# Kernel optimization log

Measured on AMD Instinct MI355X. Metric: run time of the kernel, lower is better.

Reference implementation:

```python
import jax, jax.numpy as jnp
import numpy as np

D_MODEL = 768
N_HEADS = 8
HEAD_DIM = D_MODEL // N_HEADS
LN_EPS = 1e-5

def setup_inputs() -> dict:
    key = jax.random.key(0)
    k1, k2, k3 = jax.random.split(key, 3)
    B, L = 8, 4096
    x = jax.random.normal(k1, (B, L, D_MODEL), dtype=jnp.float32)
    gamma = jnp.ones((D_MODEL,), dtype=jnp.float32)
    beta = jnp.zeros((D_MODEL,), dtype=jnp.float32)
    # torch Linear weights transposed so forward is x @ W
    w_qkv = jax.random.normal(k2, (D_MODEL, 3 * D_MODEL), dtype=jnp.float32) * (1.0 / np.sqrt(D_MODEL))
    w_out = jax.random.normal(k3, (D_MODEL, D_MODEL), dtype=jnp.float32) * (1.0 / np.sqrt(D_MODEL))
    return {"x": x, "gamma": gamma, "beta": beta, "w_qkv": w_qkv, "w_out": w_out}

def reference(x, gamma, beta, w_qkv, w_out):
    B, L, D = x.shape
    residual = x
    # LayerNorm
    mu = jnp.mean(x, axis=-1, keepdims=True)
    var = jnp.mean(jnp.square(x - mu), axis=-1, keepdims=True)
    xn = (x - mu) * jax.lax.rsqrt(var + LN_EPS) * gamma + beta
    # qkv projection, split, reshape to [B, H, L, d]
    qkv = xn @ w_qkv  # [B, L, 3D]
    q, k, v = jnp.split(qkv, 3, axis=-1)
    def to_heads(t):
        return t.reshape(B, L, N_HEADS, HEAD_DIM).transpose(0, 2, 1, 3)
    q, k, v = to_heads(q), to_heads(k), to_heads(v)
    # feature maps: elu + 1
    q = jax.nn.elu(q) + 1.0
    k = jax.nn.elu(k) + 1.0
    # linear attention: kv aggregation then query readout
    kv = jnp.einsum('bhld,bhlv->bhdv', k, v)          # [B,H,d,d]
    out = jnp.einsum('bhld,bhdv->bhlv', q, kv)         # [B,H,L,d]
    k_sum = jnp.sum(k, axis=2)                         # [B,H,d]
    normalizer = jnp.einsum('bhld,bhd->bhl', q, k_sum) # [B,H,L]
    normalizer = jnp.maximum(normalizer, 1e-6)
    out = out / normalizer[..., None]
    out = out.transpose(0, 2, 1, 3).reshape(B, L, D)
    out = out @ w_out
    return out + residual
```

## Files before the change

kernel.cpp:

```cpp
#include <hip/hip_runtime.h>
#include <stdint.h>

#define D_MODEL 768
#define N3      2304
#define NHEAD   8
#define DH      96
#define BATCH   8
#define SEQ     4096
#define ROWS    (BATCH*SEQ)
#define LN_EPS  1e-5f

typedef __attribute__((ext_vector_type(8))) __bf16 bf16x8;
typedef __attribute__((ext_vector_type(4))) float f32x4;
typedef __attribute__((ext_vector_type(8))) unsigned short ushort8;
typedef __attribute__((ext_vector_type(4))) unsigned short ushort4v;

__device__ __forceinline__ unsigned short f2bf(float f) {
  union { float f; unsigned int u; } v; v.f = f;
  unsigned int r = v.u + 0x7FFFu + ((v.u >> 16) & 1u);
  return (unsigned short)(r >> 16);
}
__device__ __forceinline__ float bf2f(unsigned short u) {
  union { unsigned int u; float f; } v; v.u = ((unsigned int)u) << 16;
  return v.f;
}

#define GLOBAL_LDS16(src, dst) \
  __builtin_amdgcn_global_load_lds((const __attribute__((address_space(1))) void*)(src), \
                                   (__attribute__((address_space(3))) void*)(dst), 16, 0, 0)

#define GATE(n) do { asm volatile("s_waitcnt vmcnt(" #n ")" ::: "memory"); \
                     __builtin_amdgcn_s_barrier(); asm volatile("" ::: "memory"); } while (0)

__global__ __launch_bounds__(256) void transpose2_kernel(
    const float* __restrict__ wqkv, const float* __restrict__ wout,
    unsigned short* __restrict__ wqkvT, unsigned short* __restrict__ woutT) {
  __shared__ float tile[32][33];
  int bx = blockIdx.x;
  const float* in; unsigned short* out; int C, c0;
  if (bx < 72) { in = wqkv; out = wqkvT; C = N3;      c0 = bx * 32; }
  else         { in = wout; out = woutT; C = D_MODEL; c0 = (bx - 72) * 32; }
  int r0 = blockIdx.y * 32;
  int tx = threadIdx.x & 31, ty = threadIdx.x >> 5;
  #pragma unroll
  for (int i = ty; i < 32; i += 8)
    tile[i][tx] = in[(size_t)(r0 + i) * C + c0 + tx];
  __syncthreads();
  #pragma unroll
  for (int i = ty; i < 32; i += 8)
    out[(size_t)(c0 + i) * D_MODEL + r0 + tx] = f2bf(tile[tx][i]);
}

__global__ __launch_bounds__(256) void ln_kernel(
    const float* __restrict__ x, const float* __restrict__ gamma,
    const float* __restrict__ beta, unsigned short* __restrict__ xn) {
  int wave = threadIdx.x >> 6, lane = threadIdx.x & 63;
  int row = blockIdx.x * 4 + wave;
  const float* xr = x + (size_t)row * D_MODEL;
  f32x4 v[3];
  float s = 0.f, sq = 0.f;
  #pragma unroll
  for (int i = 0; i < 3; ++i) {
    v[i] = *(const f32x4*)(xr + (i * 64 + lane) * 4);
    #pragma unroll
    for (int c = 0; c < 4; ++c) { s += v[i][c]; sq += v[i][c] * v[i][c]; }
  }
  #pragma unroll
  for (int o = 32; o; o >>= 1) {
    s  += __shfl_xor(s, o, 64);
    sq += __shfl_xor(sq, o, 64);
  }
  float mu  = s * (1.f / 768.f);
  float var = sq * (1.f / 768.f) - mu * mu;
  float rs  = rsqrtf(var + LN_EPS);
  #pragma unroll
  for (int i = 0; i < 3; ++i) {
    int col = (i * 64 + lane) * 4;
    ushort4v o;
    #pragma unroll
    for (int c = 0; c < 4; ++c)
      o[c] = f2bf((v[i][c] - mu) * rs * gamma[col + c] + beta[col + c]);
    *(ushort4v*)(xn + (size_t)row * D_MODEL + col) = o;
  }
}

__global__ __launch_bounds__(256, 2) void gemm_qkv_w_kernel(
    const unsigned short* __restrict__ A, const unsigned short* __restrict__ Bt,
    unsigned short* __restrict__ qb, unsigned short* __restrict__ kT,
    unsigned short* __restrict__ vT) {
  __shared__ unsigned short As[3 * 4096];
  __shared__ unsigned short Bs[3 * 8192];
  const int K = D_MODEL, nbn = 9;
  int nwg = gridDim.x, id = blockIdx.x;
  int q8 = nwg >> 3;
  int wg = (id & 7) * q8 + (id >> 3);
  int bm = wg / nbn, bn = wg % nbn;

  const int lane = threadIdx.x & 63, wid = threadIdx.x >> 6;
  const int wn = wid;
  const int l15 = lane & 15, hi = lane >> 4;
  const int colS = (hi ^ ((l15 >> 1) & 3)) << 3;
  const int srow = lane >> 2;
  const int scol = ((lane & 3) ^ ((lane >> 3) & 3)) << 3;

  const unsigned short* a0 = A  + (size_t)(bm * 128 +      wid * 16 + srow) * K + scol;
  const unsigned short* a1 = A  + (size_t)(bm * 128 + 64 + wid * 16 + srow) * K + scol;
  const unsigned short* b0 = Bt + (size_t)(bn * 256 + wid * 64 +      srow) * K + scol;
  const unsigned short* b1 = Bt + (size_t)(bn * 256 + wid * 64 + 16 + srow) * K + scol;
  const unsigned short* b2 = Bt + (size_t)(bn * 256 + wid * 64 + 32 + srow) * K + scol;
  const unsigned short* b3 = Bt + (size_t)(bn * 256 + wid * 64 + 48 + srow) * K + scol;
  auto stage = [&](int buf, int kt) {
    GLOBAL_LDS16(a0 + kt * 32, &As[buf * 4096 +        wid * 512]);
    GLOBAL_LDS16(a1 + kt * 32, &As[buf * 4096 + 2048 + wid * 512]);
    GLOBAL_LDS16(b0 + kt * 32, &Bs[buf * 8192 + wid * 2048]);
    GLOBAL_LDS16(b1 + kt * 32, &Bs[buf * 8192 + wid * 2048 + 512]);
    GLOBAL_LDS16(b2 + kt * 32, &Bs[buf * 8192 + wid * 2048 + 1024]);
    GLOBAL_LDS16(b3 + kt * 32, &Bs[buf * 8192 + wid * 2048 + 1536]);
  };

  f32x4 acc[8][4];
  #pragma unroll
  for (int i = 0; i < 8; ++i)
    #pragma unroll
    for (int j = 0; j < 4; ++j) acc[i][j] = (f32x4){0.f, 0.f, 0.f, 0.f};

#define QTILE(BUF, STG) do { \
    bf16x8 af[8], bv[4]; \
    _Pragma("unroll") for (int mf = 0; mf < 8; ++mf) \
      af[mf] = *(const bf16x8*)&As[(BUF) * 4096 + (mf * 16 + l15) * 32 + colS]; \
    _Pragma("unroll") for (int nf = 0; nf < 4; ++nf) \
      bv[nf] = *(const bf16x8*)&Bs[(BUF) * 8192 + (wn * 64 + nf * 16 + l15) * 32 + colS]; \
    STG; \
    __builtin_amdgcn_s_setprio(1); \
    _Pragma("unroll") for (int mf = 0; mf < 8; ++mf) \
      _Pragma("unroll") for (int nf = 0; nf < 4; ++nf) \
        acc[mf][nf] = __builtin_amdgcn_mfma_f32_16x16x32_bf16( \
            af[mf], bv[nf], acc[mf][nf], 0, 0, 0); \
    __builtin_amdgcn_s_setprio(0); \
  } while (0)

  stage(0, 0); stage(1, 1);
  for (int it = 0; it < 7; ++it) {
    int T = 3 * it;
    GATE(6); QTILE(0, stage(2, T + 2));
    GATE(6); QTILE(1, stage(0, T + 3));
    GATE(6); QTILE(2, stage(1, T + 4));
  }
  GATE(6); QTILE(0, stage(2, 23));
  GATE(6); QTILE(1, {});
  GATE(0); QTILE(2, {});
#undef QTILE

  int r0 = bm * 128, c0 = bn * 256 + wn * 64;
  if (bn < 3) {
    #pragma unroll
    for (int mf = 0; mf < 8; ++mf)
      #pragma unroll
      for (int nf = 0; nf < 4; ++nf) {
        int col = c0 + nf * 16 + l15;
        #pragma unroll
        for (int r = 0; r < 4; ++r) {
          int row = r0 + mf * 16 + hi * 4 + r;
          float v = acc[mf][nf][r];
          v = (v > 0.f) ? v + 1.f : __expf(v);
          qb[(size_t)row * D_MODEL + col] = f2bf(v);
        }
      }
  } else {
    const bool isK = (bn < 6);
    unsigned short* T = isK ? kT : vT;
    int cbase = c0 - (isK ? 768 : 1536);
    #pragma unroll
    for (int mf = 0; mf < 8; ++mf) {
      int ll = mf * 16 + hi * 4;
      #pragma unroll
      for (int nf = 0; nf < 4; ++nf) {
        int cc = cbase + nf * 16 + l15;
        int h = cc / 96, d = cc - h * 96;
        ushort4v pk;
        #pragma unroll
        for (int r = 0; r < 4; ++r) {
          float v = acc[mf][nf][r];
          if (isK) v = (v > 0.f) ? v + 1.f : __expf(v);
          pk[r] = f2bf(v);
        }
        *(ushort4v*)&T[(((size_t)bm * 8 + h) * 96 + d) * 128 + ll] = pk;
      }
    }
  }
}

__global__ __launch_bounds__(256) void kvagg2_kernel(
    const unsigned short* __restrict__ kT, const unsigned short* __restrict__ vT,
    float* __restrict__ kvp) {
  __shared__ unsigned short KTs[3 * 6144];
  __shared__ unsigned short VTs[3 * 8192];
  int bh = blockIdx.x >> 2, chunk = blockIdx.x & 3;
  int tid = threadIdx.x;
  int lane = tid & 63, wid = tid >> 6;
  int l15 = lane & 15, hi = lane >> 4;

  #pragma unroll
  for (int i = 0; i < 3; ++i) {
    int s = i * 256 + tid;
    int buf = s >> 8, r = 96 + ((s >> 3) & 31), sl = s & 7;
    unsigned short val = (r == 96) ? (unsigned short)0x3F80 : (unsigned short)0;
    ushort8 v8 = {val, val, val, val, val, val, val, val};
    *(ushort8*)&VTs[buf * 8192 + r * 64 + sl * 8] = v8;
  }
  __syncthreads();

  const int b = bh >> 3, h = bh & 7;
  auto stage = [&](int buf, int t) {
    #pragma unroll
    for (int i = 0; i < 3; ++i) {
      int sidx = i * 256 + tid;
      int row = sidx >> 3;
      int L = (sidx & 7) ^ (row & 7);
      size_t g = ((((size_t)b * 32 + chunk * 8 + (t >> 1)) * 8 + h) * 96 + row) * 128
               + (t & 1) * 64 + L * 8;
      GLOBAL_LDS16(kT + g, &KTs[buf * 6144 + (i * 256 + wid * 64) * 8]);
      GLOBAL_LDS16(vT + g, &VTs[buf * 8192 + (i * 256 + wid * 64) * 8]);
    }
  };

  f32x4 acc[6][2];
  #pragma unroll
  for (int i = 0; i < 6; ++i)
    #pragma unroll
    for (int j = 0; j < 2; ++j) acc[i][j] = (f32x4){0.f, 0.f, 0.f, 0.f};

#define KVTILE(BUF) do { \
    _Pragma("unroll") for (int kq = 0; kq < 2; ++kq) { \
      bf16x8 af[6], bv[2]; \
      _Pragma("unroll") for (int mf = 0; mf < 6; ++mf) { \
        int row = mf * 16 + l15; \
        af[mf] = *(const bf16x8*)&KTs[(BUF) * 6144 + row * 64 + ((kq * 4 + hi) ^ (row & 7)) * 8]; } \
      _Pragma("unroll") for (int nf = 0; nf < 2; ++nf) { \
        int row = wid * 32 + nf * 16 + l15; \
        bv[nf] = *(const bf16x8*)&VTs[(BUF) * 8192 + row * 64 + ((kq * 4 + hi) ^ (row & 7)) * 8]; } \
      __builtin_amdgcn_s_setprio(1); \
      _Pragma("unroll") for (int mf = 0; mf < 6; ++mf) \
        _Pragma("unroll") for (int nf = 0; nf < 2; ++nf) \
          acc[mf][nf] = __builtin_amdgcn_mfma_f32_16x16x32_bf16( \
              af[mf], bv[nf], acc[mf][nf], 0, 0, 0); \
      __builtin_amdgcn_s_setprio(0); \
    } } while (0)

  stage(0, 0); stage(1, 1);
  for (int t = 0; t < 14; ++t) {
    stage((t + 2) % 3, t + 2);
    GATE(12);
    KVTILE(t % 3);
  }
  GATE(6); KVTILE(2);
  GATE(0); KVTILE(0);
#undef KVTILE

  float* outp = kvp + ((size_t)bh * 4 + chunk) * (96 * 112);
  #pragma unroll
  for (int nf = 0; nf < 2; ++nf) {
    int e = wid * 32 + nf * 16 + l15;
    if (e < 112) {
      #pragma unroll
      for (int mf = 0; mf < 6; ++mf)
        #pragma unroll
        for (int r = 0; r < 4; ++r) {
          int d = mf * 16 + hi * 4 + r;
          outp[d * 112 + e] = acc[mf][nf][r];
        }
    }
  }
}

__global__ __launch_bounds__(256) void kvreduce2_kernel(
    const float* __restrict__ kvp, unsigned short* __restrict__ kvN,
    float* __restrict__ ksumf) {
  int idx = blockIdx.x * 256 + threadIdx.x;
  if (idx >= 64 * 96 * 112) return;
  int e = idx % 112;
  int d = (idx / 112) % 96;
  int bh = idx / (112 * 96);
  float s = 0.f;
  #pragma unroll
  for (int c = 0; c < 4; ++c)
    s += kvp[(((size_t)bh * 4 + c) * 96 + d) * 112 + e];
  if (e < 96)       kvN[((size_t)bh * 96 + d) * 96 + e] = f2bf(s);
  else if (e == 96) ksumf[(size_t)bh * 96 + d] = s;
}

__global__ __launch_bounds__(256) void mpre_kernel(
    const unsigned short* __restrict__ kvN, const unsigned short* __restrict__ woutT,
    unsigned short* __restrict__ Mt) {
  int bx = blockIdx.x;
  int cb = bx % 3, h = (bx / 3) % 8, b = bx / 24;
  int bh = b * 8 + h;
  const int lane = threadIdx.x & 63, wid = threadIdx.x >> 6;
  const int l15 = lane & 15, hi = lane >> 4;

  f32x4 acc[6][4];
  #pragma unroll
  for (int i = 0; i < 6; ++i)
    #pragma unroll
    for (int j = 0; j < 4; ++j) acc[i][j] = (f32x4){0.f, 0.f, 0.f, 0.f};

  #pragma unroll
  for (int kq = 0; kq < 3; ++kq) {
    int e = kq * 32 + hi * 8;
    bf16x8 af[6], bv[4];
    #pragma unroll
    for (int rf = 0; rf < 6; ++rf) {
      int d = rf * 16 + l15;
      af[rf] = *(const bf16x8*)&kvN[((size_t)bh * 96 + d) * 96 + e];
    }
    #pragma unroll
    for (int cf = 0; cf < 4; ++cf) {
      int c = cb * 256 + wid * 64 + cf * 16 + l15;
      bv[cf] = *(const bf16x8*)&woutT[(size_t)c * 768 + h * 96 + e];
    }
    #pragma unroll
    for (int rf = 0; rf < 6; ++rf)
      #pragma unroll
      for (int cf = 0; cf < 4; ++cf)
        acc[rf][cf] = __builtin_amdgcn_mfma_f32_16x16x32_bf16(
            af[rf], bv[cf], acc[rf][cf], 0, 0, 0);
  }

  #pragma unroll
  for (int rf = 0; rf < 6; ++rf) {
    int hd = h * 96 + rf * 16 + hi * 4;
    #pragma unroll
    for (int cf = 0; cf < 4; ++cf) {
      int c = cb * 256 + wid * 64 + cf * 16 + l15;
      ushort4v pk;
      #pragma unroll
      for (int r = 0; r < 4; ++r) pk[r] = f2bf(acc[rf][cf][r]);
      *(ushort4v*)&Mt[(size_t)b * 589824 + (size_t)c * 768 + hd] = pk;
    }
  }
}

__global__ __launch_bounds__(256) void scale_kernel(
    const unsigned short* __restrict__ qb, const float* __restrict__ ksumf,
    unsigned short* __restrict__ qhat) {
  __shared__ float ks[8][96];
  int tid = threadIdx.x;
  int row0 = blockIdx.x * 64;
  int b = row0 >> 12;
  #pragma unroll
  for (int i = 0; i < 3; ++i) {
    int idx = i * 256 + tid;
    if (idx < 768) ks[idx / 96][idx % 96] = ksumf[(size_t)b * 768 + idx];
  }
  __syncthreads();

  int row = row0 + (tid >> 2), seg = tid & 3;
  size_t base = (size_t)row * D_MODEL + seg * 192;
  ushort8 qreg[24];
  #pragma unroll
  for (int c = 0; c < 24; ++c)
    qreg[c] = *(const ushort8*)(qb + base + c * 8);

  float inv[2];
  #pragma unroll
  for (int hh = 0; hh < 2; ++hh) {
    int h = seg * 2 + hh;
    float n = 0.f;
    #pragma unroll
    for (int c = 0; c < 12; ++c)
      #pragma unroll
      for (int j = 0; j < 8; ++j)
        n += bf2f(qreg[hh * 12 + c][j]) * ks[h][c * 8 + j];
    inv[hh] = 1.f / fmaxf(n, 1e-6f);
  }
  #pragma unroll
  for (int c = 0; c < 24; ++c) {
    float sc = inv[c / 12];
    ushort8 o;
    #pragma unroll
    for (int j = 0; j < 8; ++j) o[j] = f2bf(bf2f(qreg[c][j]) * sc);
    *(ushort8*)(qhat + base + c * 8) = o;
  }
}

__global__ __launch_bounds__(256, 2) void gemm_fin_kernel(
    const unsigned short* __restrict__ A, const unsigned short* __restrict__ MtAll,
    const float* __restrict__ resid, float* __restrict__ Cf) {
  __shared__ unsigned short As[3 * 4096];
  __shared__ unsigned short Bs[3 * 8192];
  const int K = D_MODEL, nbn = 3;
  int nwg = gridDim.x, id = blockIdx.x;
  int q8 = nwg >> 3;
  int wg = (id & 7) * q8 + (id >> 3);
  int bm = wg / nbn, bn = wg % nbn;
  const unsigned short* Bt = MtAll + (size_t)(bm >> 5) * 589824;

  const int lane = threadIdx.x & 63, wid = threadIdx.x >> 6;
  const int wn = wid;
  const int l15 = lane & 15, hi = lane >> 4;
  const int colS = (hi ^ ((l15 >> 1) & 3)) << 3;
  const int srow = lane >> 2;
  const int scol = ((lane & 3) ^ ((lane >> 3) & 3)) << 3;

  const unsigned short* a0 = A  + (size_t)(bm * 128 +      wid * 16 + srow) * K + scol;
  const unsigned short* a1 = A  + (size_t)(bm * 128 + 64 + wid * 16 + srow) * K + scol;
  const unsigned short* b0 = Bt + (size_t)(bn * 256 + wid * 64 +      srow) * K + scol;
  const unsigned short* b1 = Bt + (size_t)(bn * 256 + wid * 64 + 16 + srow) * K + scol;
  const unsigned short* b2 = Bt + (size_t)(bn * 256 + wid * 64 + 32 + srow) * K + scol;
  const unsigned short* b3 = Bt + (size_t)(bn * 256 + wid * 64 + 48 + srow) * K + scol;
  auto stage = [&](int buf, int kt) {
    GLOBAL_LDS16(a0 + kt * 32, &As[buf * 4096 +        wid * 512]);
    GLOBAL_LDS16(a1 + kt * 32, &As[buf * 4096 + 2048 + wid * 512]);
    GLOBAL_LDS16(b0 + kt * 32, &Bs[buf * 8192 + wid * 2048]);
    GLOBAL_LDS16(b1 + kt * 32, &Bs[buf * 8192 + wid * 2048 + 512]);
    GLOBAL_LDS16(b2 + kt * 32, &Bs[buf * 8192 + wid * 2048 + 1024]);
    GLOBAL_LDS16(b3 + kt * 32, &Bs[buf * 8192 + wid * 2048 + 1536]);
  };

  f32x4 acc[8][4];
  #pragma unroll
  for (int i = 0; i < 8; ++i)
    #pragma unroll
    for (int j = 0; j < 4; ++j) acc[i][j] = (f32x4){0.f, 0.f, 0.f, 0.f};

#define FTILE(BUF, STG) do { \
    bf16x8 af[8], bv[4]; \
    _Pragma("unroll") for (int mf = 0; mf < 8; ++mf) \
      af[mf] = *(const bf16x8*)&As[(BUF) * 4096 + (mf * 16 + l15) * 32 + colS]; \
    _Pragma("unroll") for (int nf = 0; nf < 4; ++nf) \
      bv[nf] = *(const bf16x8*)&Bs[(BUF) * 8192 + (wn * 64 + nf * 16 + l15) * 32 + colS]; \
    STG; \
    __builtin_amdgcn_s_setprio(1); \
    _Pragma("unroll") for (int mf = 0; mf < 8; ++mf) \
      _Pragma("unroll") for (int nf = 0; nf < 4; ++nf) \
        acc[mf][nf] = __builtin_amdgcn_mfma_f32_16x16x32_bf16( \
            af[mf], bv[nf], acc[mf][nf], 0, 0, 0); \
    __builtin_amdgcn_s_setprio(0); \
  } while (0)

  stage(0, 0); stage(1, 1);
  for (int it = 0; it < 7; ++it) {
    int T = 3 * it;
    GATE(6); FTILE(0, stage(2, T + 2));
    GATE(6); FTILE(1, stage(0, T + 3));
    GATE(6); FTILE(2, stage(1, T + 4));
  }
  GATE(6); FTILE(0, stage(2, 23));
  GATE(6); FTILE(1, {});
  GATE(0); FTILE(2, {});
#undef FTILE

  int r0 = bm * 128, c0 = bn * 256 + wn * 64;
  #pragma unroll
  for (int mf = 0; mf < 8; ++mf)
    #pragma unroll
    for (int nf = 0; nf < 4; ++nf) {
      int col = c0 + nf * 16 + l15;
      #pragma unroll
      for (int r = 0; r < 4; ++r) {
        int row = r0 + mf * 16 + hi * 4 + r;
        Cf[(size_t)row * D_MODEL + col] =
            acc[mf][nf][r] + resid[(size_t)row * D_MODEL + col];
      }
    }
}

extern "C" void kernel_launch(void* const* d_in, const int* in_sizes, int n_in,
                              void* d_out, int out_size, void* d_ws, size_t ws_size,
                              hipStream_t stream) {
  const float* x     = (const float*)d_in[0];
  const float* gamma = (const float*)d_in[1];
  const float* beta  = (const float*)d_in[2];
  const float* w_qkv = (const float*)d_in[3];
  const float* w_out = (const float*)d_in[4];
  float* out = (float*)d_out;

  char* ws = (char*)d_ws;
  size_t off = 0;
  auto alloc = [&](size_t bytes) -> void* {
    void* p = ws + off; off += (bytes + 255) & ~(size_t)255; return p;
  };
  unsigned short* xn    = (unsigned short*)alloc((size_t)ROWS * D_MODEL * 2);
  unsigned short* qb    = (unsigned short*)alloc((size_t)ROWS * D_MODEL * 2);
  unsigned short* kTb   = (unsigned short*)alloc((size_t)64 * 96 * SEQ * 2);
  unsigned short* vTb   = (unsigned short*)alloc((size_t)64 * 96 * SEQ * 2);
  unsigned short* wqkvT = (unsigned short*)alloc((size_t)N3 * D_MODEL * 2);
  unsigned short* woutT = (unsigned short*)alloc((size_t)D_MODEL * D_MODEL * 2);
  float* kvp            = (float*)alloc((size_t)256 * 96 * 112 * 4);
  unsigned short* kvN   = (unsigned short*)alloc((size_t)64 * 96 * 96 * 2);
  float* ksumf          = (float*)alloc((size_t)64 * 96 * 4);
  unsigned short* Mt    = (unsigned short*)alloc((size_t)BATCH * 768 * 768 * 2);

  transpose2_kernel<<<dim3(96, 24), 256, 0, stream>>>(w_qkv, w_out, wqkvT, woutT);
  ln_kernel<<<ROWS / 4, 256, 0, stream>>>(x, gamma, beta, xn);
  gemm_qkv_w_kernel<<<(ROWS / 128) * (N3 / 256), 256, 0, stream>>>(xn, wqkvT, qb, kTb, vTb);
  kvagg2_kernel<<<256, 256, 0, stream>>>(kTb, vTb, kvp);
  kvreduce2_kernel<<<(64 * 96 * 112 + 255) / 256, 256, 0, stream>>>(kvp, kvN, ksumf);
  mpre_kernel<<<192, 256, 0, stream>>>(kvN, woutT, Mt);
  scale_kernel<<<ROWS / 64, 256, 0, stream>>>(qb, ksumf, xn);
  gemm_fin_kernel<<<(ROWS / 128) * 3, 256, 0, stream>>>(xn, Mt, x, out);
}
```

Baseline: 328.2 us.

## Merge independent kernels into combined launches and split kv aggregation across eight chunks

The weight transpose and LayerNorm now run in one launch, with block ranges picking the role. The Mt precompute and the q scaling kernel are merged the same way. This cuts launch count and lets independent work overlap. The kv aggregation grid doubles from 256 to 512 blocks, each doing half the sequence tiles, and the constant-one column used for k_sum moves into a small shared tile instead of padded V rows. This raises occupancy on the many CUs and shrinks LDS use, but doubles the partial buffer the reduce kernel has to read.

```diff
diff --git a/kernel.cpp b/kernel.cpp
--- a/kernel.cpp
+++ b/kernel.cpp
@@ -32,30 +32,31 @@
 #define GATE(n) do { asm volatile("s_waitcnt vmcnt(" #n ")" ::: "memory"); \
                      __builtin_amdgcn_s_barrier(); asm volatile("" ::: "memory"); } while (0)
 
-__global__ __launch_bounds__(256) void transpose2_kernel(
+__global__ __launch_bounds__(256) void prep_kernel(
     const float* __restrict__ wqkv, const float* __restrict__ wout,
-    unsigned short* __restrict__ wqkvT, unsigned short* __restrict__ woutT) {
-  __shared__ float tile[32][33];
-  int bx = blockIdx.x;
-  const float* in; unsigned short* out; int C, c0;
-  if (bx < 72) { in = wqkv; out = wqkvT; C = N3;      c0 = bx * 32; }
-  else         { in = wout; out = woutT; C = D_MODEL; c0 = (bx - 72) * 32; }
-  int r0 = blockIdx.y * 32;
-  int tx = threadIdx.x & 31, ty = threadIdx.x >> 5;
-  #pragma unroll
-  for (int i = ty; i < 32; i += 8)
-    tile[i][tx] = in[(size_t)(r0 + i) * C + c0 + tx];
-  __syncthreads();
-  #pragma unroll
-  for (int i = ty; i < 32; i += 8)
-    out[(size_t)(c0 + i) * D_MODEL + r0 + tx] = f2bf(tile[tx][i]);
-}
-
-__global__ __launch_bounds__(256) void ln_kernel(
+    unsigned short* __restrict__ wqkvT, unsigned short* __restrict__ woutT,
     const float* __restrict__ x, const float* __restrict__ gamma,
     const float* __restrict__ beta, unsigned short* __restrict__ xn) {
+  if (blockIdx.x < 2304) {
+    __shared__ float tile[32][33];
+    int v = blockIdx.x;
+    int bx = v % 96, by = v / 96;
+    const float* in; unsigned short* out; int C, c0;
+    if (bx < 72) { in = wqkv; out = wqkvT; C = N3;      c0 = bx * 32; }
+    else         { in = wout; out = woutT; C = D_MODEL; c0 = (bx - 72) * 32; }
+    int r0 = by * 32;
+    int tx = threadIdx.x & 31, ty = threadIdx.x >> 5;
+    #pragma unroll
+    for (int i = ty; i < 32; i += 8)
+      tile[i][tx] = in[(size_t)(r0 + i) * C + c0 + tx];
+    __syncthreads();
+    #pragma unroll
+    for (int i = ty; i < 32; i += 8)
+      out[(size_t)(c0 + i) * D_MODEL + r0 + tx] = f2bf(tile[tx][i]);
+    return;
+  }
   int wave = threadIdx.x >> 6, lane = threadIdx.x & 63;
-  int row = blockIdx.x * 4 + wave;
+  int row = (blockIdx.x - 2304) * 4 + wave;
   const float* xr = x + (size_t)row * D_MODEL;
   f32x4 v[3];
   float s = 0.f, sq = 0.f;
@@ -190,23 +191,22 @@
   }
 }
 
-__global__ __launch_bounds__(256) void kvagg2_kernel(
+__global__ __launch_bounds__(256) void kvagg3_kernel(
     const unsigned short* __restrict__ kT, const unsigned short* __restrict__ vT,
     float* __restrict__ kvp) {
   __shared__ unsigned short KTs[3 * 6144];
-  __shared__ unsigned short VTs[3 * 8192];
-  int bh = blockIdx.x >> 2, chunk = blockIdx.x & 3;
+  __shared__ unsigned short VTs[3 * 6144];
+  __shared__ unsigned short PH[2048];
+  int bh = blockIdx.x >> 3, chunk = blockIdx.x & 7;
   int tid = threadIdx.x;
   int lane = tid & 63, wid = tid >> 6;
   int l15 = lane & 15, hi = lane >> 4;
 
-  #pragma unroll
-  for (int i = 0; i < 3; ++i) {
-    int s = i * 256 + tid;
-    int buf = s >> 8, r = 96 + ((s >> 3) & 31), sl = s & 7;
-    unsigned short val = (r == 96) ? (unsigned short)0x3F80 : (unsigned short)0;
+  {
+    int r = tid >> 3, sl = tid & 7;
+    unsigned short val = (r == 0) ? (unsigned short)0x3F80 : (unsigned short)0;
     ushort8 v8 = {val, val, val, val, val, val, val, val};
-    *(ushort8*)&VTs[buf * 8192 + r * 64 + sl * 8] = v8;
+    *(ushort8*)&PH[(r * 8 + sl) * 8] = v8;
   }
   __syncthreads();
 
@@ -217,10 +217,10 @@
       int sidx = i * 256 + tid;
       int row = sidx >> 3;
       int L = (sidx & 7) ^ (row & 7);
-      size_t g = ((((size_t)b * 32 + chunk * 8 + (t >> 1)) * 8 + h) * 96 + row) * 128
+      size_t g = ((((size_t)b * 32 + chunk * 4 + (t >> 1)) * 8 + h) * 96 + row) * 128
                + (t & 1) * 64 + L * 8;
       GLOBAL_LDS16(kT + g, &KTs[buf * 6144 + (i * 256 + wid * 64) * 8]);
-      GLOBAL_LDS16(vT + g, &VTs[buf * 8192 + (i * 256 + wid * 64) * 8]);
+      GLOBAL_LDS16(vT + g, &VTs[buf * 6144 + (i * 256 + wid * 64) * 8]);
     }
   };
 
@@ -236,9 +236,15 @@
       _Pragma("unroll") for (int mf = 0; mf < 6; ++mf) { \
         int row = mf * 16 + l15; \
         af[mf] = *(const bf16x8*)&KTs[(BUF) * 6144 + row * 64 + ((kq * 4 + hi) ^ (row & 7)) * 8]; } \
-      _Pragma("unroll") for (int nf = 0; nf < 2; ++nf) { \
-        int row = wid * 32 + nf * 16 + l15; \
-        bv[nf] = *(const bf16x8*)&VTs[(BUF) * 8192 + row * 64 + ((kq * 4 + hi) ^ (row & 7)) * 8]; } \
+      if (wid < 3) { \
+        _Pragma("unroll") for (int nf = 0; nf < 2; ++nf) { \
+          int row = wid * 32 + nf * 16 + l15; \
+          bv[nf] = *(const bf16x8*)&VTs[(BUF) * 6144 + row * 64 + ((kq * 4 + hi) ^ (row & 7)) * 8]; } \
+      } else { \
+        _Pragma("unroll") for (int nf = 0; nf < 2; ++nf) { \
+          int row = nf * 16 + l15; \
+          bv[nf] = *(const bf16x8*)&PH[row * 64 + ((kq * 4 + hi) ^ ((row + 96) & 7)) * 8]; } \
+      } \
       __builtin_amdgcn_s_setprio(1); \
       _Pragma("unroll") for (int mf = 0; mf < 6; ++mf) \
         _Pragma("unroll") for (int nf = 0; nf < 2; ++nf) \
@@ -248,16 +254,16 @@
     } } while (0)
 
   stage(0, 0); stage(1, 1);
-  for (int t = 0; t < 14; ++t) {
+  for (int t = 0; t < 6; ++t) {
     stage((t + 2) % 3, t + 2);
     GATE(12);
     KVTILE(t % 3);
   }
-  GATE(6); KVTILE(2);
-  GATE(0); KVTILE(0);
+  GATE(6); KVTILE(0);
+  GATE(0); KVTILE(1);
 #undef KVTILE
 
-  float* outp = kvp + ((size_t)bh * 4 + chunk) * (96 * 112);
+  float* outp = kvp + ((size_t)bh * 8 + chunk) * (96 * 112);
   #pragma unroll
   for (int nf = 0; nf < 2; ++nf) {
     int e = wid * 32 + nf * 16 + l15;
@@ -283,69 +289,69 @@
   int bh = idx / (112 * 96);
   float s = 0.f;
   #pragma unroll
-  for (int c = 0; c < 4; ++c)
-    s += kvp[(((size_t)bh * 4 + c) * 96 + d) * 112 + e];
+  for (int c = 0; c < 8; ++c)
+    s += kvp[(((size_t)bh * 8 + c) * 96 + d) * 112 + e];
   if (e < 96)       kvN[((size_t)bh * 96 + d) * 96 + e] = f2bf(s);
   else if (e == 96) ksumf[(size_t)bh * 96 + d] = s;
 }
 
-__global__ __launch_bounds__(256) void mpre_kernel(
+__global__ __launch_bounds__(256) void mid_kernel(
     const unsigned short* __restrict__ kvN, const unsigned short* __restrict__ woutT,
-    unsigned short* __restrict__ Mt) {
-  int bx = blockIdx.x;
-  int cb = bx % 3, h = (bx / 3) % 8, b = bx / 24;
-  int bh = b * 8 + h;
-  const int lane = threadIdx.x & 63, wid = threadIdx.x >> 6;
-  const int l15 = lane & 15, hi = lane >> 4;
-
-  f32x4 acc[6][4];
-  #pragma unroll
-  for (int i = 0; i < 6; ++i)
-    #pragma unroll
-    for (int j = 0; j < 4; ++j) acc[i][j] = (f32x4){0.f, 0.f, 0.f, 0.f};
-
-  #pragma unroll
-  for (int kq = 0; kq < 3; ++kq) {
-    int e = kq * 32 + hi * 8;
-    bf16x8 af[6], bv[4];
-    #pragma unroll
-    for (int rf = 0; rf < 6; ++rf) {
-      int d = rf * 16 + l15;
-      af[rf] = *(const bf16x8*)&kvN[((size_t)bh * 96 + d) * 96 + e];
-    }
-    #pragma unroll
-    for (int cf = 0; cf < 4; ++cf) {
-      int c = cb * 256 + wid * 64 + cf * 16 + l15;
-      bv[cf] = *(const bf16x8*)&woutT[(size_t)c * 768 + h * 96 + e];
-    }
-    #pragma unroll
-    for (int rf = 0; rf < 6; ++rf)
-      #pragma unroll
-      for (int cf = 0; cf < 4; ++cf)
-        acc[rf][cf] = __builtin_amdgcn_mfma_f32_16x16x32_bf16(
-            af[rf], bv[cf], acc[rf][cf], 0, 0, 0);
-  }
-
-  #pragma unroll
-  for (int rf = 0; rf < 6; ++rf) {
-    int hd = h * 96 + rf * 16 + hi * 4;
-    #pragma unroll
-    for (int cf = 0; cf < 4; ++cf) {
-      int c = cb * 256 + wid * 64 + cf * 16 + l15;
-      ushort4v pk;
-      #pragma unroll
-      for (int r = 0; r < 4; ++r) pk[r] = f2bf(acc[rf][cf][r]);
-      *(ushort4v*)&Mt[(size_t)b * 589824 + (size_t)c * 768 + hd] = pk;
-    }
-  }
-}
-
-__global__ __launch_bounds__(256) void scale_kernel(
+    unsigned short* __restrict__ Mt,
     const unsigned short* __restrict__ qb, const float* __restrict__ ksumf,
     unsigned short* __restrict__ qhat) {
+  if (blockIdx.x < 192) {
+    int bx = blockIdx.x;
+    int cb = bx % 3, h = (bx / 3) % 8, b = bx / 24;
+    int bh = b * 8 + h;
+    const int lane = threadIdx.x & 63, wid = threadIdx.x >> 6;
+    const int l15 = lane & 15, hi = lane >> 4;
+
+    f32x4 acc[6][4];
+    #pragma unroll
+    for (int i = 0; i < 6; ++i)
+      #pragma unroll
+      for (int j = 0; j < 4; ++j) acc[i][j] = (f32x4){0.f, 0.f, 0.f, 0.f};
+
+    #pragma unroll
+    for (int kq = 0; kq < 3; ++kq) {
+      int e = kq * 32 + hi * 8;
+      bf16x8 af[6], bv[4];
+      #pragma unroll
+      for (int rf = 0; rf < 6; ++rf) {
+        int d = rf * 16 + l15;
+        af[rf] = *(const bf16x8*)&kvN[((size_t)bh * 96 + d) * 96 + e];
+      }
+      #pragma unroll
+      for (int cf = 0; cf < 4; ++cf) {
+        int c = cb * 256 + wid * 64 + cf * 16 + l15;
+        bv[cf] = *(const bf16x8*)&woutT[(size_t)c * 768 + h * 96 + e];
+      }
+      #pragma unroll
+      for (int rf = 0; rf < 6; ++rf)
+        #pragma unroll
+        for (int cf = 0; cf < 4; ++cf)
+          acc[rf][cf] = __builtin_amdgcn_mfma_f32_16x16x32_bf16(
+              af[rf], bv[cf], acc[rf][cf], 0, 0, 0);
+    }
+
+    #pragma unroll
+    for (int rf = 0; rf < 6; ++rf) {
+      int hd = h * 96 + rf * 16 + hi * 4;
+      #pragma unroll
+      for (int cf = 0; cf < 4; ++cf) {
+        int c = cb * 256 + wid * 64 + cf * 16 + l15;
+        ushort4v pk;
+        #pragma unroll
+        for (int r = 0; r < 4; ++r) pk[r] = f2bf(acc[rf][cf][r]);
+        *(ushort4v*)&Mt[(size_t)b * 589824 + (size_t)c * 768 + hd] = pk;
+      }
+    }
+    return;
+  }
   __shared__ float ks[8][96];
   int tid = threadIdx.x;
-  int row0 = blockIdx.x * 64;
+  int row0 = (blockIdx.x - 192) * 64;
   int b = row0 >> 12;
   #pragma unroll
   for (int i = 0; i < 3; ++i) {
@@ -486,17 +492,16 @@
   unsigned short* vTb   = (unsigned short*)alloc((size_t)64 * 96 * SEQ * 2);
   unsigned short* wqkvT = (unsigned short*)alloc((size_t)N3 * D_MODEL * 2);
   unsigned short* woutT = (unsigned short*)alloc((size_t)D_MODEL * D_MODEL * 2);
-  float* kvp            = (float*)alloc((size_t)256 * 96 * 112 * 4);
+  float* kvp            = (float*)alloc((size_t)512 * 96 * 112 * 4);
   unsigned short* kvN   = (unsigned short*)alloc((size_t)64 * 96 * 96 * 2);
   float* ksumf          = (float*)alloc((size_t)64 * 96 * 4);
   unsigned short* Mt    = (unsigned short*)alloc((size_t)BATCH * 768 * 768 * 2);
 
-  transpose2_kernel<<<dim3(96, 24), 256, 0, stream>>>(w_qkv, w_out, wqkvT, woutT);
-  ln_kernel<<<ROWS / 4, 256, 0, stream>>>(x, gamma, beta, xn);
+  prep_kernel<<<2304 + ROWS / 4, 256, 0, stream>>>(w_qkv, w_out, wqkvT, woutT,
+                                                   x, gamma, beta, xn);
   gemm_qkv_w_kernel<<<(ROWS / 128) * (N3 / 256), 256, 0, stream>>>(xn, wqkvT, qb, kTb, vTb);
-  kvagg2_kernel<<<256, 256, 0, stream>>>(kTb, vTb, kvp);
+  kvagg3_kernel<<<512, 256, 0, stream>>>(kTb, vTb, kvp);
   kvreduce2_kernel<<<(64 * 96 * 112 + 255) / 256, 256, 0, stream>>>(kvp, kvN, ksumf);
-  mpre_kernel<<<192, 256, 0, stream>>>(kvN, woutT, Mt);
-  scale_kernel<<<ROWS / 64, 256, 0, stream>>>(qb, ksumf, xn);
+  mid_kernel<<<192 + ROWS / 64, 256, 0, stream>>>(kvN, woutT, Mt, qb, ksumf, xn);
   gemm_fin_kernel<<<(ROWS / 128) * 3, 256, 0, stream>>>(xn, Mt, x, out);
 }
```

Measured after the change: 312.2 us, median of 2. 4.9% less time.
